# Optimization experiments

Measured on AMD Instinct MI355X. Metric: run time of the kernel, lower is better.

## Reference

```python
import jax, jax.numpy as jnp
import numpy as np

B, T, D, H = 8, 1024, 512, 8
HD = D // H  # per-head hidden = embed_dim // n_head = 64
EPS = 1e-5


def setup_inputs() -> dict:
    key = jax.random.key(0)
    ks = jax.random.split(key, 8)
    x = jax.random.normal(ks[0], (B, T, D), dtype=jnp.float32)
    sc = 1.0 / np.sqrt(D)
    Wq = jax.random.normal(ks[1], (D, H * HD), dtype=jnp.float32) * sc
    Wk = jax.random.normal(ks[2], (D, H * HD), dtype=jnp.float32) * sc
    Wp = jax.random.normal(ks[3], (H * HD, D), dtype=jnp.float32) * sc
    bq = jnp.zeros((H * HD,), jnp.float32)
    bk = jnp.zeros((H * HD,), jnp.float32)
    bp = jnp.zeros((D,), jnp.float32)
    w_mlp = jax.random.normal(ks[4], (2 * HD,), dtype=jnp.float32) * 0.1
    ln_g = jnp.ones((D,), jnp.float32)
    ln_b = jnp.zeros((D,), jnp.float32)
    return {"x": x, "Wq": Wq, "bq": bq, "Wk": Wk, "bk": bk,
            "Wp": Wp, "bp": bp, "w_mlp": w_mlp, "ln_g": ln_g, "ln_b": ln_b}


def reference(x, Wq, bq, Wk, bk, Wp, bp, w_mlp, ln_g, ln_b):
    b, t, d = x.shape
    h, hd = H, HD
    # q/k projections, split into heads: [B,T,H,hd]
    qx = (x @ Wq + bq).reshape(b, t, h, hd)
    kx = (x @ Wk + bk).reshape(b, t, h, hd)
    # MLP score: tanh(concat(k_j, q_i) . w) == tanh(k_j.w[:hd] + q_i.w[hd:])
    k_s = jnp.einsum('bkhd,d->bkh', kx, w_mlp[:hd])   # [B,K,H]
    q_s = jnp.einsum('bqhd,d->bqh', qx, w_mlp[hd:])   # [B,Q,H]
    score = jnp.tanh(q_s[:, :, None, :] + k_s[:, None, :, :])  # [B,Q,K,H]
    attn = jax.nn.softmax(score, axis=2)  # softmax over k_len
    # values are the key projection kx (bmm(score, kx) in original)
    out = jnp.einsum('bqkh,bkhd->bqhd', attn, kx).reshape(b, t, h * hd)
    out = out @ Wp + bp  # output projection (dropout is identity at eval)
    # residual + LayerNorm
    y = x + out
    mu = jnp.mean(y, axis=-1, keepdims=True)
    var = jnp.var(y, axis=-1, keepdims=True)
    yn = (y - mu) * jax.lax.rsqrt(var + EPS)
    return yn * ln_g + ln_b
```

## Files before the change

### kernel.cpp

```cpp
#include <hip/hip_runtime.h>
#include <cstddef>

#define TT 1024
#define DDIM 512
#define HH 8
#define NND 128
#define NS 68

typedef __attribute__((ext_vector_type(8))) short bfrag;
typedef __attribute__((ext_vector_type(4))) float facc;

#define SC2   2.8853900817779268f
#define L2E   1.4426950408889634f

static __device__ __forceinline__ unsigned bfrne(float f) {
    unsigned u = __float_as_uint(f);
    return (u + 0x7fffu + ((u >> 16) & 1u)) >> 16;
}
static __device__ __forceinline__ unsigned pack2rne(float a, float b) {
    return bfrne(a) | (bfrne(b) << 16);
}
static __device__ __forceinline__ unsigned pack2hu(float a, float b) {
    return ((__float_as_uint(a) + 0x8000u) >> 16) |
           ((__float_as_uint(b) + 0x8000u) & 0xffff0000u);
}
static __device__ __forceinline__ void gl2lds16(const void* g, void* l) {
    __builtin_amdgcn_global_load_lds(
        (const __attribute__((address_space(1))) unsigned int*)g,
        (__attribute__((address_space(3))) unsigned int*)l, 16, 0, 0);
}
static __device__ __forceinline__ float wt(float t) {
    float r = __builtin_amdgcn_rcpf(t + 1.f);
    return __builtin_amdgcn_exp2f(fmaf(r, -2.f * L2E, L2E));
}

__global__ __launch_bounds__(256) void prepare_kernel(
    const float* __restrict__ x, const float* __restrict__ Wk,
    const float* __restrict__ Wp, const float* __restrict__ Wq,
    const float* __restrict__ bq, const float* __restrict__ wm,
    unsigned short* __restrict__ xb, unsigned short* __restrict__ WkT,
    unsigned short* __restrict__ WpT, unsigned short* __restrict__ vq2b,
    float* __restrict__ qsb2)
{
    const int bx = blockIdx.x, tid = threadIdx.x;
    const int lane = tid & 63, wave = tid >> 6;
    if (bx < 2048) {
        const int row = bx * 4 + wave;
        const float4* xr = (const float4*)(x + (size_t)row * DDIM);
        float4 x0 = xr[lane * 2], x1 = xr[lane * 2 + 1];
        uint4 st;
        st.x = pack2rne(x0.x, x0.y); st.y = pack2rne(x0.z, x0.w);
        st.z = pack2rne(x1.x, x1.y); st.w = pack2rne(x1.z, x1.w);
        int p = lane ^ (row & 7);
        *(uint4*)(xb + (size_t)row * DDIM + p * 8) = st;
    } else if (bx < 2176) {
        int idx = bx - 2048;
        const float* src = (idx & 64) ? Wp : Wk;
        unsigned short* dst = (idx & 64) ? WpT : WkT;
        idx &= 63;
        const int n0 = (idx & 7) * 64, k0 = (idx >> 3) * 64;
        __shared__ float sT[64][65];
        #pragma unroll
        for (int it = 0; it < 4; ++it) {
            int task = it * 256 + tid;
            int kr = task >> 4, c4 = (task & 15) * 4;
            float4 v = *(const float4*)(src + (size_t)(k0 + kr) * DDIM + n0 + c4);
            sT[kr][c4] = v.x; sT[kr][c4 + 1] = v.y; sT[kr][c4 + 2] = v.z; sT[kr][c4 + 3] = v.w;
        }
        __syncthreads();
        #pragma unroll
        for (int it = 0; it < 2; ++it) {
            int task = it * 256 + tid;
            int n = task >> 3, kg = task & 7;
            unsigned u[4];
            #pragma unroll
            for (int jj = 0; jj < 4; ++jj)
                u[jj] = pack2rne(sT[kg * 8 + jj * 2][n], sT[kg * 8 + jj * 2 + 1][n]);
            int p = ((k0 >> 3) + kg) ^ (n & 7);
            uint4 st; st.x = u[0]; st.y = u[1]; st.z = u[2]; st.w = u[3];
            *(uint4*)(dst + (size_t)(n0 + n) * DDIM + p * 8) = st;
        }
    } else {
        int idx = (bx - 2176) * 4 + wave;
        int h = idx >> 9, d = idx & 511;
        float v = Wq[(size_t)d * DDIM + h * 64 + lane] * wm[64 + lane];
        #pragma unroll
        for (int off = 32; off > 0; off >>= 1) v += __shfl_xor(v, off);
        if (lane == 0) vq2b[h * DDIM + d] = (unsigned short)bfrne(v * SC2);
        if (bx == 2176 && tid < HH) {
            float sb = 0.f;
            for (int j = 0; j < 64; ++j)
                sb = fmaf(bq[tid * 64 + j], wm[64 + j], sb);
            qsb2[tid] = sb * SC2;
        }
    }
}

__global__ __launch_bounds__(256) void gemm1_kernel(
    const unsigned short* __restrict__ A, const unsigned short* __restrict__ B,
    const float* __restrict__ bias, unsigned short* __restrict__ kxTg,
    float* __restrict__ ks2, const float* __restrict__ wm,
    const unsigned short* __restrict__ vq2b, const float* __restrict__ qsb2,
    float* __restrict__ qs2)
{
    __shared__ __align__(16) unsigned short smem[50176];
    unsigned short* svq = smem + 49152;
    const int tid = threadIdx.x, lane = tid & 63, wave = tid >> 6;
    const int l15 = lane & 15, quad = lane >> 4;
    const int wr = wave >> 1, wc = wave & 1;
    const int row0 = blockIdx.x * 128, colpair = blockIdx.y;
    const int h = colpair * 2 + wc, n0 = colpair * 128;

    const float qsbh = qsb2[h];
    float bvv[4], wmv[4];
    #pragma unroll
    for (int nt = 0; nt < 4; ++nt) {
        bvv[nt] = bias[h * 64 + nt * 16 + l15];
        wmv[nt] = wm[nt * 16 + l15] * SC2;
    }

    facc acc[4][4]; facc accq[4];
    #pragma unroll
    for (int i = 0; i < 4; ++i) {
        #pragma unroll
        for (int j = 0; j < 4; ++j) { acc[i][j][0]=0.f; acc[i][j][1]=0.f; acc[i][j][2]=0.f; acc[i][j][3]=0.f; }
        accq[i][0]=0.f; accq[i][1]=0.f; accq[i][2]=0.f; accq[i][3]=0.f;
    }

    if (tid < 128)
        gl2lds16(vq2b + colpair * 1024 + tid * 8, &svq[tid * 8]);

    auto stage = [&](int sel, int k0) {
        unsigned short* dA = smem + sel * 16384;
        unsigned short* dB = dA + 8192;
        #pragma unroll
        for (int it = 0; it < 4; ++it) {
            int g = it * 256 + tid;
            int r = g >> 3, kg = g & 7;
            gl2lds16(A + (size_t)(row0 + r) * 512 + k0 + kg * 8, &dA[g * 8]);
            gl2lds16(B + (size_t)(n0 + r) * 512 + k0 + kg * 8, &dB[g * 8]);
        }
    };

    stage(0, 0);
    stage(1, 64);
    #pragma unroll
    for (int kt = 0; kt < 8; ++kt) {
        const int sel = kt % 3;
        if (kt < 6) {
            stage((kt + 2) % 3, (kt + 2) * 64);
            asm volatile("s_waitcnt vmcnt(16)" ::: "memory");
        } else if (kt == 6) {
            asm volatile("s_waitcnt vmcnt(8)" ::: "memory");
        } else {
            asm volatile("s_waitcnt vmcnt(0)" ::: "memory");
        }
        __builtin_amdgcn_s_barrier();
        __builtin_amdgcn_sched_barrier(0);
        const unsigned short* sA = smem + sel * 16384;
        const unsigned short* sB = sA + 8192;
        #pragma unroll
        for (int ks_ = 0; ks_ < 2; ++ks_) {
            int slot = (ks_ * 4 + quad) ^ (l15 & 7);
            bfrag a[4], b[4];
            #pragma unroll
            for (int i = 0; i < 4; ++i) {
                a[i] = *(const bfrag*)&sA[(wr * 64 + i * 16 + l15) * 64 + slot * 8];
                b[i] = *(const bfrag*)&sB[(wc * 64 + i * 16 + l15) * 64 + slot * 8];
            }
            bfrag bvq = *(const bfrag*)&svq[wc * 512 + kt * 64 + ks_ * 32 + quad * 8];
            #pragma unroll
            for (int i = 0; i < 4; ++i) {
                #pragma unroll
                for (int nt = 0; nt < 4; ++nt)
                    acc[i][nt] = __builtin_amdgcn_mfma_f32_16x16x32_bf16(a[i], b[nt], acc[i][nt], 0, 0, 0);
                accq[i] = __builtin_amdgcn_mfma_f32_16x16x32_bf16(a[i], bvq, accq[i], 0, 0, 0);
            }
        }
        __builtin_amdgcn_s_barrier();
        __builtin_amdgcn_sched_barrier(0);
    }
    asm volatile("" ::: "memory");

    const int bb = row0 >> 10, t0 = row0 & 1023;
    float part[4][4];
    #pragma unroll
    for (int i = 0; i < 4; ++i)
        #pragma unroll
        for (int r = 0; r < 4; ++r) part[i][r] = 0.f;

    unsigned short* eT = smem + wc * 8704;
    #pragma unroll
    for (int i = 0; i < 4; ++i) {
        int tr = wr * 64 + i * 16 + quad * 4;
        #pragma unroll
        for (int nt = 0; nt < 4; ++nt) {
            int d = nt * 16 + l15;
            float v0 = acc[i][nt][0] + bvv[nt], v1 = acc[i][nt][1] + bvv[nt];
            float v2 = acc[i][nt][2] + bvv[nt], v3 = acc[i][nt][3] + bvv[nt];
            part[i][0] = fmaf(wmv[nt], v0, part[i][0]);
            part[i][1] = fmaf(wmv[nt], v1, part[i][1]);
            part[i][2] = fmaf(wmv[nt], v2, part[i][2]);
            part[i][3] = fmaf(wmv[nt], v3, part[i][3]);
            *(unsigned*)&eT[d * 136 + tr]     = pack2rne(v0, v1);
            *(unsigned*)&eT[d * 136 + tr + 2] = pack2rne(v2, v3);
        }
    }
    #pragma unroll
    for (int i = 0; i < 4; ++i)
        #pragma unroll
        for (int r = 0; r < 4; ++r) {
            float p = part[i][r];
            p += __shfl_xor(p, 1); p += __shfl_xor(p, 2);
            p += __shfl_xor(p, 4); p += __shfl_xor(p, 8);
            if (l15 == 0) {
                size_t o = (size_t)(bb * HH + h) * TT + t0 + wr * 64 + i * 16 + quad * 4 + r;
                ks2[o] = p;
                qs2[o] = accq[i][r] + qsbh;
            }
        }
    __syncthreads();
    #pragma unroll
    for (int it = 0; it < 8; ++it) {
        int task = it * 256 + tid;
        int hh = task >> 10, rem = task & 1023;
        int col = rem >> 4, seg = rem & 15;
        uint4 v = *(const uint4*)&smem[hh * 8704 + col * 136 + seg * 8];
        int hg = colpair * 2 + hh;
        int g = (t0 >> 3) + seg;
        int p = g ^ (col & 7);
        *(uint4*)(kxTg + ((size_t)(bb * HH + hg) * 64 + col) * TT + p * 8) = v;
    }
}

__global__ __launch_bounds__(256) void nodes_kernel(
    const unsigned short* __restrict__ kxTg, const float* __restrict__ qs2,
    const float* __restrict__ ks2, float* __restrict__ npart)
{
    __shared__ __align__(16) unsigned short kxT[16384];
    __shared__ float tks[256];
    __shared__ float redl[8];
    const int bh = blockIdx.x, kq = blockIdx.y;
    const int tid = threadIdx.x, lane = tid & 63, wave = tid >> 6;
    const int l15 = lane & 15, quad = lane >> 4;
    const unsigned short* kxbase = kxTg + (size_t)bh * 64 * TT;

    #pragma unroll
    for (int it = 0; it < 8; ++it) {
        int g = it * 256 + tid;
        int d = g >> 5, j = g & 31;
        gl2lds16(kxbase + (size_t)d * TT + kq * 256 + j * 8, &kxT[g * 8]);
    }
    float ksv = ks2[(size_t)bh * TT + kq * 256 + tid];
    float4 q4 = ((const float4*)(qs2 + (size_t)bh * TT))[tid];
    tks[tid] = __builtin_amdgcn_exp2f(ksv);
    float mn = fminf(fminf(q4.x, q4.y), fminf(q4.z, q4.w));
    float mx = fmaxf(fmaxf(q4.x, q4.y), fmaxf(q4.z, q4.w));
    #pragma unroll
    for (int off = 32; off > 0; off >>= 1) {
        mn = fminf(mn, __shfl_xor(mn, off));
        mx = fmaxf(mx, __shfl_xor(mx, off));
    }
    if (lane == 0) { redl[wave] = mn; redl[4 + wave] = mx; }
    __syncthreads();
    const float mnv = fminf(fminf(redl[0], redl[1]), fminf(redl[2], redl[3]));
    const float mxv = fmaxf(fmaxf(redl[4], redl[5]), fmaxf(redl[6], redl[7]));
    const float h2v = (mxv - mnv) * (1.f / 127.f);
    const float zA = mnv + (wave * 16 + l15) * h2v;
    const float zB = zA + 64.f * h2v;
    const float tzA = __builtin_amdgcn_exp2f(zA);
    const float tzB = __builtin_amdgcn_exp2f(zB);

    facc acc[2][4]; facc accZ[2];
    #pragma unroll
    for (int g = 0; g < 2; ++g) {
        #pragma unroll
        for (int i = 0; i < 4; ++i) { acc[g][i][0]=0.f; acc[g][i][1]=0.f; acc[g][i][2]=0.f; acc[g][i][3]=0.f; }
        accZ[g][0]=0.f; accZ[g][1]=0.f; accZ[g][2]=0.f; accZ[g][3]=0.f;
    }
    bfrag ones;
    #pragma unroll
    for (int j = 0; j < 8; ++j) ones[j] = (short)0x3F80;

    #pragma unroll
    for (int kst = 0; kst < 8; ++kst) {
        const float* kvp = &tks[kst * 32 + quad * 8];
        float4 kv0 = *(const float4*)kvp;
        float4 kv1 = *(const float4*)(kvp + 4);
        int slot = (kst * 4 + quad) ^ (l15 & 7);
        bfrag bf_[4];
        #pragma unroll
        for (int dt = 0; dt < 4; ++dt)
            bf_[dt] = *(const bfrag*)&kxT[(dt * 16 + l15) * 256 + slot * 8];
        #pragma unroll
        for (int g = 0; g < 2; ++g) {
            float tz = g ? tzB : tzA;
            union { unsigned u[4]; bfrag f; } afu;
            afu.u[0] = pack2hu(wt(tz * kv0.x), wt(tz * kv0.y));
            afu.u[1] = pack2hu(wt(tz * kv0.z), wt(tz * kv0.w));
            afu.u[2] = pack2hu(wt(tz * kv1.x), wt(tz * kv1.y));
            afu.u[3] = pack2hu(wt(tz * kv1.z), wt(tz * kv1.w));
            #pragma unroll
            for (int dt = 0; dt < 4; ++dt)
                acc[g][dt] = __builtin_amdgcn_mfma_f32_16x16x32_bf16(afu.f, bf_[dt], acc[g][dt], 0, 0, 0);
            accZ[g] = __builtin_amdgcn_mfma_f32_16x16x32_bf16(afu.f, ones, accZ[g], 0, 0, 0);
        }
    }
    float* dst = npart + (size_t)(bh * 4 + kq) * (NND * NS);
    #pragma unroll
    for (int g = 0; g < 2; ++g)
        #pragma unroll
        for (int r = 0; r < 4; ++r) {
            int node = g * 64 + wave * 16 + quad * 4 + r;
            #pragma unroll
            for (int dt = 0; dt < 4; ++dt)
                dst[node * NS + dt * 16 + l15] = acc[g][dt][r];
            if (l15 == 0) dst[node * NS + 64] = accZ[g][r];
        }
}

__global__ __launch_bounds__(256) void interp_kernel(
    const float* __restrict__ npart, const float* __restrict__ qs2,
    unsigned short* __restrict__ attb)
{
    __shared__ __align__(16) float nodes[NND * NS];
    __shared__ float redl[8];
    const int bh = blockIdx.x, tq = blockIdx.y;
    const int b = bh >> 3, h = bh & 7;
    const int tid = threadIdx.x, lane = tid & 63, wave = tid >> 6;

    float4 q4 = ((const float4*)(qs2 + (size_t)bh * TT))[tid];
    float mn = fminf(fminf(q4.x, q4.y), fminf(q4.z, q4.w));
    float mx = fmaxf(fmaxf(q4.x, q4.y), fmaxf(q4.z, q4.w));
    #pragma unroll
    for (int off = 32; off > 0; off >>= 1) {
        mn = fminf(mn, __shfl_xor(mn, off));
        mx = fmaxf(mx, __shfl_xor(mx, off));
    }
    if (lane == 0) { redl[wave] = mn; redl[4 + wave] = mx; }
    __syncthreads();
    const float mnv = fminf(fminf(redl[0], redl[1]), fminf(redl[2], redl[3]));
    const float mxv = fmaxf(fmaxf(redl[4], redl[5]), fmaxf(redl[6], redl[7]));
    const float inv127v = 127.f / fmaxf(mxv - mnv, 1e-12f);

    const float4* p0 = (const float4*)(npart + (size_t)(bh * 4 + 0) * (NND * NS));
    const float4* p1 = (const float4*)(npart + (size_t)(bh * 4 + 1) * (NND * NS));
    const float4* p2 = (const float4*)(npart + (size_t)(bh * 4 + 2) * (NND * NS));
    const float4* p3 = (const float4*)(npart + (size_t)(bh * 4 + 3) * (NND * NS));
    #pragma unroll
    for (int it = 0; it < 9; ++it) {
        int g = it * 256 + tid;
        if (g < (NND * NS) / 4) {
            float4 a = p0[g], bb4 = p1[g], c = p2[g], d = p3[g];
            float4 s;
            s.x = a.x + bb4.x + c.x + d.x;
            s.y = a.y + bb4.y + c.y + d.y;
            s.z = a.z + bb4.z + c.z + d.z;
            s.w = a.w + bb4.w + c.w + d.w;
            ((float4*)nodes)[g] = s;
        }
    }
    __syncthreads();

    const float* qsp = qs2 + (size_t)bh * TT;
    #pragma unroll 2
    for (int it = 0; it < 16; ++it) {
        int task = it * 256 + tid;
        int t = tq * 256 + (task >> 4), dp = task & 15;
        float qv = qsp[t];
        float u = (qv - mnv) * inv127v;
        int i = (int)floorf(u) - 1;
        i = i < 0 ? 0 : (i > NND - 4 ? NND - 4 : i);
        float s = u - (float)i;
        float s1 = s - 1.f, s2 = s - 2.f, s3 = s - 3.f;
        float w0 = -s1 * s2 * s3 * (1.f / 6.f);
        float w1 = s * s2 * s3 * 0.5f;
        float w2 = -s * s1 * s3 * 0.5f;
        float w3 = s * s1 * s2 * (1.f / 6.f);
        const float* base = &nodes[i * NS];
        float4 v0 = *(const float4*)(base + 4 * dp);
        float4 v1 = *(const float4*)(base + NS + 4 * dp);
        float4 v2 = *(const float4*)(base + 2 * NS + 4 * dp);
        float4 v3 = *(const float4*)(base + 3 * NS + 4 * dp);
        float zz = w0 * base[64] + w1 * base[NS + 64] + w2 * base[2 * NS + 64] + w3 * base[3 * NS + 64];
        float ox = w0 * v0.x + w1 * v1.x + w2 * v2.x + w3 * v3.x;
        float oy = w0 * v0.y + w1 * v1.y + w2 * v2.y + w3 * v3.y;
        float oz = w0 * v0.z + w1 * v1.z + w2 * v2.z + w3 * v3.z;
        float ow = w0 * v0.w + w1 * v1.w + w2 * v2.w + w3 * v3.w;
        float rz = __builtin_amdgcn_rcpf(zz);
        uint2 st;
        st.x = pack2rne(ox * rz, oy * rz);
        st.y = pack2rne(oz * rz, ow * rz);
        int row = b * TT + t;
        int col = h * 64 + 4 * dp;
        int p = (col >> 3) ^ (row & 7);
        *(uint2*)&attb[(size_t)row * DDIM + p * 8 + (col & 7)] = st;
    }
}

__global__ __launch_bounds__(256) void gemm2_kernel(
    const unsigned short* __restrict__ A, const unsigned short* __restrict__ B,
    const float* __restrict__ bias, unsigned short* __restrict__ yb)
{
    __shared__ __align__(16) unsigned short smem[49152];
    const int tid = threadIdx.x, lane = tid & 63, wave = tid >> 6;
    const int l15 = lane & 15, quad = lane >> 4;
    const int wr = wave >> 1, wc = wave & 1;
    const int row0 = blockIdx.x * 128, col0 = blockIdx.y * 128;

    float bvv[4];
    #pragma unroll
    for (int nt = 0; nt < 4; ++nt) bvv[nt] = bias[col0 + wc * 64 + nt * 16 + l15];

    facc acc[4][4];
    #pragma unroll
    for (int i = 0; i < 4; ++i)
        #pragma unroll
        for (int j = 0; j < 4; ++j) { acc[i][j][0]=0.f; acc[i][j][1]=0.f; acc[i][j][2]=0.f; acc[i][j][3]=0.f; }

    auto stage = [&](int sel, int k0) {
        unsigned short* dA = smem + sel * 16384;
        unsigned short* dB = dA + 8192;
        #pragma unroll
        for (int it = 0; it < 4; ++it) {
            int g = it * 256 + tid;
            int r = g >> 3, kg = g & 7;
            gl2lds16(A + (size_t)(row0 + r) * 512 + k0 + kg * 8, &dA[g * 8]);
            gl2lds16(B + (size_t)(col0 + r) * 512 + k0 + kg * 8, &dB[g * 8]);
        }
    };

    stage(0, 0);
    stage(1, 64);
    #pragma unroll
    for (int kt = 0; kt < 8; ++kt) {
        const int sel = kt % 3;
        if (kt < 6) {
            stage((kt + 2) % 3, (kt + 2) * 64);
            asm volatile("s_waitcnt vmcnt(16)" ::: "memory");
        } else if (kt == 6) {
            asm volatile("s_waitcnt vmcnt(8)" ::: "memory");
        } else {
            asm volatile("s_waitcnt vmcnt(0)" ::: "memory");
        }
        __builtin_amdgcn_s_barrier();
        __builtin_amdgcn_sched_barrier(0);
        const unsigned short* sA = smem + sel * 16384;
        const unsigned short* sB = sA + 8192;
        #pragma unroll
        for (int ks_ = 0; ks_ < 2; ++ks_) {
            int slot = (ks_ * 4 + quad) ^ (l15 & 7);
            bfrag a[4], b[4];
            #pragma unroll
            for (int i = 0; i < 4; ++i) {
                a[i] = *(const bfrag*)&sA[(wr * 64 + i * 16 + l15) * 64 + slot * 8];
                b[i] = *(const bfrag*)&sB[(wc * 64 + i * 16 + l15) * 64 + slot * 8];
            }
            #pragma unroll
            for (int i = 0; i < 4; ++i)
                #pragma unroll
                for (int nt = 0; nt < 4; ++nt)
                    acc[i][nt] = __builtin_amdgcn_mfma_f32_16x16x32_bf16(a[i], b[nt], acc[i][nt], 0, 0, 0);
        }
        __builtin_amdgcn_s_barrier();
        __builtin_amdgcn_sched_barrier(0);
    }
    asm volatile("" ::: "memory");

    unsigned short* yT = smem;
    #pragma unroll
    for (int i = 0; i < 4; ++i) {
        #pragma unroll
        for (int nt = 0; nt < 4; ++nt) {
            int col = wc * 64 + nt * 16 + l15;
            #pragma unroll
            for (int r = 0; r < 4; ++r) {
                int row = wr * 64 + i * 16 + quad * 4 + r;
                yT[row * 136 + col] = (unsigned short)bfrne(acc[i][nt][r] + bvv[nt]);
            }
        }
    }
    __syncthreads();
    #pragma unroll
    for (int it = 0; it < 8; ++it) {
        int task = it * 256 + tid;
        int row = task >> 4, seg = task & 15;
        uint4 v = *(const uint4*)&yT[row * 136 + seg * 8];
        *(uint4*)(yb + (size_t)(row0 + row) * DDIM + col0 + seg * 8) = v;
    }
}

__global__ __launch_bounds__(256) void ln_kernel(
    const unsigned short* __restrict__ yb, const unsigned short* __restrict__ xb,
    const float* __restrict__ g, const float* __restrict__ bet,
    float* __restrict__ out)
{
    const int tid = threadIdx.x, lane = tid & 63, wave = tid >> 6;
    const int row = blockIdx.x * 4 + wave;
    uint4 pv = *(const uint4*)(yb + (size_t)row * DDIM + lane * 8);
    int pgr = lane ^ (row & 7);
    uint4 xv = *(const uint4*)(xb + (size_t)row * DDIM + pgr * 8);
    float y[8];
    const unsigned* pu = (const unsigned*)&pv;
    const unsigned* xu = (const unsigned*)&xv;
    #pragma unroll
    for (int j = 0; j < 4; ++j) {
        y[2*j]   = __uint_as_float(pu[j] << 16)        + __uint_as_float(xu[j] << 16);
        y[2*j+1] = __uint_as_float(pu[j] & 0xffff0000u) + __uint_as_float(xu[j] & 0xffff0000u);
    }
    float s = 0.f, s2 = 0.f;
    #pragma unroll
    for (int i = 0; i < 8; ++i) { s += y[i]; s2 = fmaf(y[i], y[i], s2); }
    #pragma unroll
    for (int off = 32; off > 0; off >>= 1) {
        s += __shfl_xor(s, off);
        s2 += __shfl_xor(s2, off);
    }
    float mu = s * (1.f / 512.f);
    float var = s2 * (1.f / 512.f) - mu * mu;
    float inv = rsqrtf(var + 1e-5f);
    const float4* gp = (const float4*)(g + lane * 8);
    const float4* bp = (const float4*)(bet + lane * 8);
    float4 g0 = gp[0], g1 = gp[1], b0 = bp[0], b1 = bp[1];
    float4 o0, o1;
    o0.x = (y[0] - mu) * inv * g0.x + b0.x; o0.y = (y[1] - mu) * inv * g0.y + b0.y;
    o0.z = (y[2] - mu) * inv * g0.z + b0.z; o0.w = (y[3] - mu) * inv * g0.w + b0.w;
    o1.x = (y[4] - mu) * inv * g1.x + b1.x; o1.y = (y[5] - mu) * inv * g1.y + b1.y;
    o1.z = (y[6] - mu) * inv * g1.z + b1.z; o1.w = (y[7] - mu) * inv * g1.w + b1.w;
    float4* op = (float4*)(out + (size_t)row * DDIM);
    op[lane * 2] = o0; op[lane * 2 + 1] = o1;
}

extern "C" void kernel_launch(void* const* d_in, const int* in_sizes, int n_in,
                              void* d_out, int out_size, void* d_ws, size_t ws_size,
                              hipStream_t stream)
{
    const float* x    = (const float*)d_in[0];
    const float* Wq   = (const float*)d_in[1];
    const float* bq   = (const float*)d_in[2];
    const float* Wk   = (const float*)d_in[3];
    const float* bk   = (const float*)d_in[4];
    const float* Wp   = (const float*)d_in[5];
    const float* bp   = (const float*)d_in[6];
    const float* wm   = (const float*)d_in[7];
    const float* ln_g = (const float*)d_in[8];
    const float* ln_b = (const float*)d_in[9];
    float* out = (float*)d_out;

    float* ws = (float*)d_ws;
    float*          qsb2 = ws;
    unsigned short* vq2b = (unsigned short*)(ws + 64);
    unsigned short* WkT  = (unsigned short*)(ws + 2112);
    unsigned short* WpT  = (unsigned short*)(ws + 133184);
    unsigned short* xb   = (unsigned short*)(ws + 264256);
    unsigned short* kxTg = (unsigned short*)(ws + 2361408);
    float*          qs2  = ws + 4458560;
    float*          ks2  = ws + 4524096;
    unsigned short* attb = (unsigned short*)(ws + 4589632);
    unsigned short* yb   = (unsigned short*)(ws + 6686784);
    float*          npart = ws + 8783936;

    prepare_kernel<<<3200, 256, 0, stream>>>(x, Wk, Wp, Wq, bq, wm,
                                             xb, WkT, WpT, vq2b, qsb2);
    gemm1_kernel<<<dim3(64, 4), 256, 0, stream>>>(xb, WkT, bk, kxTg, ks2, wm,
                                                  vq2b, qsb2, qs2);
    nodes_kernel<<<dim3(64, 4), 256, 0, stream>>>(kxTg, qs2, ks2, npart);
    interp_kernel<<<dim3(64, 4), 256, 0, stream>>>(npart, qs2, attb);
    gemm2_kernel<<<dim3(64, 4), 256, 0, stream>>>(attb, WpT, bp, yb);
    ln_kernel<<<2048, 256, 0, stream>>>(yb, xb, ln_g, ln_b, out);
}
```

Measured before the change: 131.3 us.

## Double waves per GEMM block and split nodes kernel across more key chunks

Both GEMM kernels move from 4 to 8 waves per block, with each wave covering half the columns, and from triple to double buffering so LDS use shrinks. In gemm1 the k-score partial sums are now combined across wave pairs through shared memory. The nodes kernel splits the key dimension into 8 chunks of 128 instead of 4 of 256, and interp sums 8 partials. The aim is more parallelism and latency hiding on a 256-block grid, at the cost of shallower prefetch, extra reduction traffic and extra syncs.

```diff
diff --git a/kernel.cpp b/kernel.cpp
--- a/kernel.cpp
+++ b/kernel.cpp
@@ -96,34 +96,35 @@
     }
 }
 
-__global__ __launch_bounds__(256) void gemm1_kernel(
+__global__ __launch_bounds__(512) void gemm1_kernel(
     const unsigned short* __restrict__ A, const unsigned short* __restrict__ B,
     const float* __restrict__ bias, unsigned short* __restrict__ kxTg,
     float* __restrict__ ks2, const float* __restrict__ wm,
     const unsigned short* __restrict__ vq2b, const float* __restrict__ qsb2,
     float* __restrict__ qs2)
 {
-    __shared__ __align__(16) unsigned short smem[50176];
-    unsigned short* svq = smem + 49152;
+    __shared__ __align__(16) unsigned short smem[33792];
+    unsigned short* svq = smem + 32768;
     const int tid = threadIdx.x, lane = tid & 63, wave = tid >> 6;
     const int l15 = lane & 15, quad = lane >> 4;
-    const int wr = wave >> 1, wc = wave & 1;
+    const int wr = wave >> 2, wc = wave & 3;
     const int row0 = blockIdx.x * 128, colpair = blockIdx.y;
-    const int h = colpair * 2 + wc, n0 = colpair * 128;
+    const int h = colpair * 2 + (wc >> 1), n0 = colpair * 128;
+    const int dofs = (wc & 1) * 32;
 
     const float qsbh = qsb2[h];
-    float bvv[4], wmv[4];
-    #pragma unroll
-    for (int nt = 0; nt < 4; ++nt) {
-        bvv[nt] = bias[h * 64 + nt * 16 + l15];
-        wmv[nt] = wm[nt * 16 + l15] * SC2;
-    }
-
-    facc acc[4][4]; facc accq[4];
+    float bvv[2], wmv[2];
+    #pragma unroll
+    for (int nt = 0; nt < 2; ++nt) {
+        bvv[nt] = bias[h * 64 + dofs + nt * 16 + l15];
+        wmv[nt] = wm[dofs + nt * 16 + l15] * SC2;
+    }
+
+    facc acc[4][2]; facc accq[4];
     #pragma unroll
     for (int i = 0; i < 4; ++i) {
         #pragma unroll
-        for (int j = 0; j < 4; ++j) { acc[i][j][0]=0.f; acc[i][j][1]=0.f; acc[i][j][2]=0.f; acc[i][j][3]=0.f; }
+        for (int j = 0; j < 2; ++j) { acc[i][j][0]=0.f; acc[i][j][1]=0.f; acc[i][j][2]=0.f; acc[i][j][3]=0.f; }
         accq[i][0]=0.f; accq[i][1]=0.f; accq[i][2]=0.f; accq[i][3]=0.f;
     }
 
@@ -134,8 +135,8 @@
         unsigned short* dA = smem + sel * 16384;
         unsigned short* dB = dA + 8192;
         #pragma unroll
-        for (int it = 0; it < 4; ++it) {
-            int g = it * 256 + tid;
+        for (int it = 0; it < 2; ++it) {
+            int g = it * 512 + tid;
             int r = g >> 3, kg = g & 7;
             gl2lds16(A + (size_t)(row0 + r) * 512 + k0 + kg * 8, &dA[g * 8]);
             gl2lds16(B + (size_t)(n0 + r) * 512 + k0 + kg * 8, &dB[g * 8]);
@@ -143,15 +144,12 @@
     };
 
     stage(0, 0);
-    stage(1, 64);
     #pragma unroll
     for (int kt = 0; kt < 8; ++kt) {
-        const int sel = kt % 3;
-        if (kt < 6) {
-            stage((kt + 2) % 3, (kt + 2) * 64);
-            asm volatile("s_waitcnt vmcnt(16)" ::: "memory");
-        } else if (kt == 6) {
-            asm volatile("s_waitcnt vmcnt(8)" ::: "memory");
+        const int sel = kt & 1;
+        if (kt < 7) {
+            stage(sel ^ 1, (kt + 1) * 64);
+            asm volatile("s_waitcnt vmcnt(4)" ::: "memory");
         } else {
             asm volatile("s_waitcnt vmcnt(0)" ::: "memory");
         }
@@ -162,19 +160,21 @@
         #pragma unroll
         for (int ks_ = 0; ks_ < 2; ++ks_) {
             int slot = (ks_ * 4 + quad) ^ (l15 & 7);
-            bfrag a[4], b[4];
-            #pragma unroll
-            for (int i = 0; i < 4; ++i) {
+            bfrag a[4], b[2];
+            #pragma unroll
+            for (int i = 0; i < 4; ++i)
                 a[i] = *(const bfrag*)&sA[(wr * 64 + i * 16 + l15) * 64 + slot * 8];
-                b[i] = *(const bfrag*)&sB[(wc * 64 + i * 16 + l15) * 64 + slot * 8];
-            }
-            bfrag bvq = *(const bfrag*)&svq[wc * 512 + kt * 64 + ks_ * 32 + quad * 8];
+            #pragma unroll
+            for (int nt = 0; nt < 2; ++nt)
+                b[nt] = *(const bfrag*)&sB[(wc * 32 + nt * 16 + l15) * 64 + slot * 8];
+            bfrag bvq = *(const bfrag*)&svq[(wc >> 1) * 512 + kt * 64 + ks_ * 32 + quad * 8];
             #pragma unroll
             for (int i = 0; i < 4; ++i) {
                 #pragma unroll
-                for (int nt = 0; nt < 4; ++nt)
+                for (int nt = 0; nt < 2; ++nt)
                     acc[i][nt] = __builtin_amdgcn_mfma_f32_16x16x32_bf16(a[i], b[nt], acc[i][nt], 0, 0, 0);
-                accq[i] = __builtin_amdgcn_mfma_f32_16x16x32_bf16(a[i], bvq, accq[i], 0, 0, 0);
+                if ((wc & 1) == 0)
+                    accq[i] = __builtin_amdgcn_mfma_f32_16x16x32_bf16(a[i], bvq, accq[i], 0, 0, 0);
             }
         }
         __builtin_amdgcn_s_barrier();
@@ -189,13 +189,13 @@
         #pragma unroll
         for (int r = 0; r < 4; ++r) part[i][r] = 0.f;
 
-    unsigned short* eT = smem + wc * 8704;
+    unsigned short* eT = smem + (wc >> 1) * 8704;
     #pragma unroll
     for (int i = 0; i < 4; ++i) {
         int tr = wr * 64 + i * 16 + quad * 4;
         #pragma unroll
-        for (int nt = 0; nt < 4; ++nt) {
-            int d = nt * 16 + l15;
+        for (int nt = 0; nt < 2; ++nt) {
+            int d = dofs + nt * 16 + l15;
             float v0 = acc[i][nt][0] + bvv[nt], v1 = acc[i][nt][1] + bvv[nt];
             float v2 = acc[i][nt][2] + bvv[nt], v3 = acc[i][nt][3] + bvv[nt];
             part[i][0] = fmaf(wmv[nt], v0, part[i][0]);
@@ -206,6 +206,7 @@
             *(unsigned*)&eT[d * 136 + tr + 2] = pack2rne(v2, v3);
         }
     }
+    float* sred = (float*)(smem + 17408);
     #pragma unroll
     for (int i = 0; i < 4; ++i)
         #pragma unroll
@@ -213,16 +214,32 @@
             float p = part[i][r];
             p += __shfl_xor(p, 1); p += __shfl_xor(p, 2);
             p += __shfl_xor(p, 4); p += __shfl_xor(p, 8);
-            if (l15 == 0) {
-                size_t o = (size_t)(bb * HH + h) * TT + t0 + wr * 64 + i * 16 + quad * 4 + r;
-                ks2[o] = p;
-                qs2[o] = accq[i][r] + qsbh;
-            }
-        }
+            part[i][r] = p;
+        }
+    if (wc & 1) {
+        #pragma unroll
+        for (int i = 0; i < 4; ++i)
+            #pragma unroll
+            for (int r = 0; r < 4; ++r)
+                if (l15 == 0) sred[(wave >> 1) * 64 + i * 16 + quad * 4 + r] = part[i][r];
+    }
     __syncthreads();
-    #pragma unroll
-    for (int it = 0; it < 8; ++it) {
-        int task = it * 256 + tid;
+    if ((wc & 1) == 0) {
+        #pragma unroll
+        for (int i = 0; i < 4; ++i)
+            #pragma unroll
+            for (int r = 0; r < 4; ++r)
+                if (l15 == 0) {
+                    float p = part[i][r] + sred[(wave >> 1) * 64 + i * 16 + quad * 4 + r];
+                    size_t o = (size_t)(bb * HH + h) * TT + t0 + wr * 64 + i * 16 + quad * 4 + r;
+                    ks2[o] = p;
+                    qs2[o] = accq[i][r] + qsbh;
+                }
+    }
+    __syncthreads();
+    #pragma unroll
+    for (int it = 0; it < 4; ++it) {
+        int task = it * 512 + tid;
         int hh = task >> 10, rem = task & 1023;
         int col = rem >> 4, seg = rem & 15;
         uint4 v = *(const uint4*)&smem[hh * 8704 + col * 136 + seg * 8];
@@ -237,8 +254,8 @@
     const unsigned short* __restrict__ kxTg, const float* __restrict__ qs2,
     const float* __restrict__ ks2, float* __restrict__ npart)
 {
-    __shared__ __align__(16) unsigned short kxT[16384];
-    __shared__ float tks[256];
+    __shared__ __align__(16) unsigned short kxT[8192];
+    __shared__ float tks[128];
     __shared__ float redl[8];
     const int bh = blockIdx.x, kq = blockIdx.y;
     const int tid = threadIdx.x, lane = tid & 63, wave = tid >> 6;
@@ -246,14 +263,14 @@
     const unsigned short* kxbase = kxTg + (size_t)bh * 64 * TT;
 
     #pragma unroll
-    for (int it = 0; it < 8; ++it) {
+    for (int it = 0; it < 4; ++it) {
         int g = it * 256 + tid;
-        int d = g >> 5, j = g & 31;
-        gl2lds16(kxbase + (size_t)d * TT + kq * 256 + j * 8, &kxT[g * 8]);
-    }
-    float ksv = ks2[(size_t)bh * TT + kq * 256 + tid];
+        int d = g >> 4, j = g & 15;
+        gl2lds16(kxbase + (size_t)d * TT + kq * 128 + j * 8, &kxT[g * 8]);
+    }
+    if (tid < 128)
+        tks[tid] = __builtin_amdgcn_exp2f(ks2[(size_t)bh * TT + kq * 128 + tid]);
     float4 q4 = ((const float4*)(qs2 + (size_t)bh * TT))[tid];
-    tks[tid] = __builtin_amdgcn_exp2f(ksv);
     float mn = fminf(fminf(q4.x, q4.y), fminf(q4.z, q4.w));
     float mx = fmaxf(fmaxf(q4.x, q4.y), fmaxf(q4.z, q4.w));
     #pragma unroll
@@ -283,7 +300,7 @@
     for (int j = 0; j < 8; ++j) ones[j] = (short)0x3F80;
 
     #pragma unroll
-    for (int kst = 0; kst < 8; ++kst) {
+    for (int kst = 0; kst < 4; ++kst) {
         const float* kvp = &tks[kst * 32 + quad * 8];
         float4 kv0 = *(const float4*)kvp;
         float4 kv1 = *(const float4*)(kvp + 4);
@@ -291,7 +308,7 @@
         bfrag bf_[4];
         #pragma unroll
         for (int dt = 0; dt < 4; ++dt)
-            bf_[dt] = *(const bfrag*)&kxT[(dt * 16 + l15) * 256 + slot * 8];
+            bf_[dt] = *(const bfrag*)&kxT[(dt * 16 + l15) * 128 + slot * 8];
         #pragma unroll
         for (int g = 0; g < 2; ++g) {
             float tz = g ? tzB : tzA;
@@ -306,7 +323,7 @@
             accZ[g] = __builtin_amdgcn_mfma_f32_16x16x32_bf16(afu.f, ones, accZ[g], 0, 0, 0);
         }
     }
-    float* dst = npart + (size_t)(bh * 4 + kq) * (NND * NS);
+    float* dst = npart + (size_t)(bh * 8 + kq) * (NND * NS);
     #pragma unroll
     for (int g = 0; g < 2; ++g)
         #pragma unroll
@@ -343,20 +360,17 @@
     const float mxv = fmaxf(fmaxf(redl[4], redl[5]), fmaxf(redl[6], redl[7]));
     const float inv127v = 127.f / fmaxf(mxv - mnv, 1e-12f);
 
-    const float4* p0 = (const float4*)(npart + (size_t)(bh * 4 + 0) * (NND * NS));
-    const float4* p1 = (const float4*)(npart + (size_t)(bh * 4 + 1) * (NND * NS));
-    const float4* p2 = (const float4*)(npart + (size_t)(bh * 4 + 2) * (NND * NS));
-    const float4* p3 = (const float4*)(npart + (size_t)(bh * 4 + 3) * (NND * NS));
+    const float* pb = npart + (size_t)(bh * 8) * (NND * NS);
     #pragma unroll
     for (int it = 0; it < 9; ++it) {
         int g = it * 256 + tid;
         if (g < (NND * NS) / 4) {
-            float4 a = p0[g], bb4 = p1[g], c = p2[g], d = p3[g];
-            float4 s;
-            s.x = a.x + bb4.x + c.x + d.x;
-            s.y = a.y + bb4.y + c.y + d.y;
-            s.z = a.z + bb4.z + c.z + d.z;
-            s.w = a.w + bb4.w + c.w + d.w;
+            float4 s = ((const float4*)pb)[g];
+            #pragma unroll
+            for (int j = 1; j < 8; ++j) {
+                float4 v = ((const float4*)(pb + (size_t)j * (NND * NS)))[g];
+                s.x += v.x; s.y += v.y; s.z += v.z; s.w += v.w;
+            }
             ((float4*)nodes)[g] = s;
         }
     }
@@ -398,32 +412,32 @@
     }
 }
 
-__global__ __launch_bounds__(256) void gemm2_kernel(
+__global__ __launch_bounds__(512) void gemm2_kernel(
     const unsigned short* __restrict__ A, const unsigned short* __restrict__ B,
     const float* __restrict__ bias, unsigned short* __restrict__ yb)
 {
-    __shared__ __align__(16) unsigned short smem[49152];
+    __shared__ __align__(16) unsigned short smem[32768];
     const int tid = threadIdx.x, lane = tid & 63, wave = tid >> 6;
     const int l15 = lane & 15, quad = lane >> 4;
-    const int wr = wave >> 1, wc = wave & 1;
+    const int wr = wave >> 2, wc = wave & 3;
     const int row0 = blockIdx.x * 128, col0 = blockIdx.y * 128;
 
-    float bvv[4];
-    #pragma unroll
-    for (int nt = 0; nt < 4; ++nt) bvv[nt] = bias[col0 + wc * 64 + nt * 16 + l15];
-
-    facc acc[4][4];
+    float bvv[2];
+    #pragma unroll
+    for (int nt = 0; nt < 2; ++nt) bvv[nt] = bias[col0 + wc * 32 + nt * 16 + l15];
+
+    facc acc[4][2];
     #pragma unroll
     for (int i = 0; i < 4; ++i)
         #pragma unroll
-        for (int j = 0; j < 4; ++j) { acc[i][j][0]=0.f; acc[i][j][1]=0.f; acc[i][j][2]=0.f; acc[i][j][3]=0.f; }
+        for (int j = 0; j < 2; ++j) { acc[i][j][0]=0.f; acc[i][j][1]=0.f; acc[i][j][2]=0.f; acc[i][j][3]=0.f; }
 
     auto stage = [&](int sel, int k0) {
         unsigned short* dA = smem + sel * 16384;
         unsigned short* dB = dA + 8192;
         #pragma unroll
-        for (int it = 0; it < 4; ++it) {
-            int g = it * 256 + tid;
+        for (int it = 0; it < 2; ++it) {
+            int g = it * 512 + tid;
             int r = g >> 3, kg = g & 7;
             gl2lds16(A + (size_t)(row0 + r) * 512 + k0 + kg * 8, &dA[g * 8]);
             gl2lds16(B + (size_t)(col0 + r) * 512 + k0 + kg * 8, &dB[g * 8]);
@@ -431,15 +445,12 @@
     };
 
     stage(0, 0);
-    stage(1, 64);
     #pragma unroll
     for (int kt = 0; kt < 8; ++kt) {
-        const int sel = kt % 3;
-        if (kt < 6) {
-            stage((kt + 2) % 3, (kt + 2) * 64);
-            asm volatile("s_waitcnt vmcnt(16)" ::: "memory");
-        } else if (kt == 6) {
-            asm volatile("s_waitcnt vmcnt(8)" ::: "memory");
+        const int sel = kt & 1;
+        if (kt < 7) {
+            stage(sel ^ 1, (kt + 1) * 64);
+            asm volatile("s_waitcnt vmcnt(4)" ::: "memory");
         } else {
             asm volatile("s_waitcnt vmcnt(0)" ::: "memory");
         }
@@ -450,16 +461,17 @@
         #pragma unroll
         for (int ks_ = 0; ks_ < 2; ++ks_) {
             int slot = (ks_ * 4 + quad) ^ (l15 & 7);
-            bfrag a[4], b[4];
-            #pragma unroll
-            for (int i = 0; i < 4; ++i) {
+            bfrag a[4], b[2];
+            #pragma unroll
+            for (int i = 0; i < 4; ++i)
                 a[i] = *(const bfrag*)&sA[(wr * 64 + i * 16 + l15) * 64 + slot * 8];
-                b[i] = *(const bfrag*)&sB[(wc * 64 + i * 16 + l15) * 64 + slot * 8];
-            }
+            #pragma unroll
+            for (int nt = 0; nt < 2; ++nt)
+                b[nt] = *(const bfrag*)&sB[(wc * 32 + nt * 16 + l15) * 64 + slot * 8];
             #pragma unroll
             for (int i = 0; i < 4; ++i)
                 #pragma unroll
-                for (int nt = 0; nt < 4; ++nt)
+                for (int nt = 0; nt < 2; ++nt)
                     acc[i][nt] = __builtin_amdgcn_mfma_f32_16x16x32_bf16(a[i], b[nt], acc[i][nt], 0, 0, 0);
         }
         __builtin_amdgcn_s_barrier();
@@ -471,8 +483,8 @@
     #pragma unroll
     for (int i = 0; i < 4; ++i) {
         #pragma unroll
-        for (int nt = 0; nt < 4; ++nt) {
-            int col = wc * 64 + nt * 16 + l15;
+        for (int nt = 0; nt < 2; ++nt) {
+            int col = wc * 32 + nt * 16 + l15;
             #pragma unroll
             for (int r = 0; r < 4; ++r) {
                 int row = wr * 64 + i * 16 + quad * 4 + r;
@@ -482,8 +494,8 @@
     }
     __syncthreads();
     #pragma unroll
-    for (int it = 0; it < 8; ++it) {
-        int task = it * 256 + tid;
+    for (int it = 0; it < 4; ++it) {
+        int task = it * 512 + tid;
         int row = task >> 4, seg = task & 15;
         uint4 v = *(const uint4*)&yT[row * 136 + seg * 8];
         *(uint4*)(yb + (size_t)(row0 + row) * DDIM + col0 + seg * 8) = v;
@@ -562,10 +574,10 @@
 
     prepare_kernel<<<3200, 256, 0, stream>>>(x, Wk, Wp, Wq, bq, wm,
                                              xb, WkT, WpT, vq2b, qsb2);
-    gemm1_kernel<<<dim3(64, 4), 256, 0, stream>>>(xb, WkT, bk, kxTg, ks2, wm,
+    gemm1_kernel<<<dim3(64, 4), 512, 0, stream>>>(xb, WkT, bk, kxTg, ks2, wm,
                                                   vq2b, qsb2, qs2);
-    nodes_kernel<<<dim3(64, 4), 256, 0, stream>>>(kxTg, qs2, ks2, npart);
+    nodes_kernel<<<dim3(64, 8), 256, 0, stream>>>(kxTg, qs2, ks2, npart);
     interp_kernel<<<dim3(64, 4), 256, 0, stream>>>(npart, qs2, attb);
-    gemm2_kernel<<<dim3(64, 4), 256, 0, stream>>>(attb, WpT, bp, yb);
+    gemm2_kernel<<<dim3(64, 4), 512, 0, stream>>>(attb, WpT, bp, yb);
     ln_kernel<<<2048, 256, 0, stream>>>(yb, xb, ln_g, ln_b, out);
 }
```

New measurement: 139.1 us. +5.9%, slower.
